# Kernel optimization log

Measured on AMD Instinct MI355X. Metric: run time of the kernel, lower is better.

Reference implementation:

```python
import jax, jax.numpy as jnp
import numpy as np

T, B, H = 2048, 64, 256   # time, batch, hidden/input/memory size
A = 256                   # attention_size
IN = H + H                # cell input size = input_size + memory_size = 512
NEG = -1e12


def setup_inputs() -> dict:
    key = jax.random.key(0)
    ks = jax.random.split(key, 12)
    s = lambda k, shape, fan: jax.random.normal(k, shape, jnp.float32) / np.sqrt(fan)
    inp = {
        "input": jax.random.normal(ks[0], (B, H), jnp.float32),
        "memory": jax.random.normal(ks[1], (T, B, H), jnp.float32),
        "memory_mask": jax.random.bernoulli(ks[2], 0.9, (T, B)),
        "state": jax.random.normal(ks[3], (B, H), jnp.float32),
        # attention MLP: Linear(input+state+memory -> A, no bias), Tanh, Linear(A -> 1, no bias)
        "W_a1": s(ks[4], (H + H + H, A), H * 3),
        "w_a2": s(ks[5], (A,), A),
        # gate: Linear(IN -> IN, no bias) + sigmoid
        "W_gate": s(ks[6], (IN, IN), IN),
        # GRUCell params (torch layout: [3H, in], gates order r,z,n)
        "W_ih": s(ks[7], (3 * H, IN), IN),
        "W_hh": s(ks[8], (3 * H, H), H),
        "b_ih": jnp.zeros((3 * H,), jnp.float32),
        "b_hh": jnp.zeros((3 * H,), jnp.float32),
    }
    return inp


def reference(input, memory, memory_mask, state, W_a1, w_a2, W_gate, W_ih, W_hh, b_ih, b_hh):
    # --- additive attention: tanh(W1 @ [input, state, memory]) @ w2 ---
    # split W_a1 by the concat layout [input | state | memory]
    qs = jnp.concatenate([input, state], axis=-1) @ W_a1[: 2 * H]      # [B, A]
    mp = jnp.einsum("tbh,ha->tba", memory, W_a1[2 * H :])               # [T, B, A]
    logits = jnp.tanh(qs[None] + mp) @ w_a2                              # [T, B]
    logits = jnp.where(memory_mask, logits, NEG)
    scores = jax.nn.softmax(logits, axis=0)                              # [T, B]
    attn_vec = jnp.einsum("tb,tbh->bh", scores, memory)                  # [B, H]

    # --- gate ---
    new_input = jnp.concatenate([input, attn_vec], axis=-1)              # [B, 2H]
    gated = new_input * jax.nn.sigmoid(new_input @ W_gate)

    # --- GRU cell (torch semantics, gates r, z, n) ---
    gi = gated @ W_ih.T + b_ih                                           # [B, 3H]
    gh = state @ W_hh.T + b_hh                                           # [B, 3H]
    i_r, i_z, i_n = jnp.split(gi, 3, axis=-1)
    h_r, h_z, h_n = jnp.split(gh, 3, axis=-1)
    r = jax.nn.sigmoid(i_r + h_r)
    z = jax.nn.sigmoid(i_z + h_z)
    n = jnp.tanh(i_n + r * h_n)
    return (1.0 - z) * n + z * state                                     # [B, H]
```

## Files before the change

kernel.cpp:

```cpp
#include <hip/hip_runtime.h>
#include <hip/hip_bf16.h>

#define B_DIM 64
#define H_DIM 256
#define NG 256
#define SUBS 8
#define RCH 64
#define NEG_INF -1e12f

typedef __attribute__((ext_vector_type(8))) short short8;
typedef __attribute__((ext_vector_type(4))) float f32x4;

__device__ __forceinline__ unsigned short bfbits(float f) {
    __hip_bfloat16 h = __float2bfloat16(f);
    unsigned short u;
    __builtin_memcpy(&u, &h, 2);
    return u;
}
__device__ __forceinline__ float fast_tanh(float x) {
    float e = __expf(2.0f * x);
    return 1.0f - 2.0f / (e + 1.0f);
}
__device__ __forceinline__ float fast_sigmoid(float x) {
    return 1.0f / (1.0f + __expf(-x));
}

__global__ void prep_qs_kernel(const float* __restrict__ W_a1,
                               const float* __restrict__ input,
                               const float* __restrict__ state,
                               unsigned short* __restrict__ WmT,
                               float* __restrict__ qs) {
    __shared__ float cat[512];
    int bid = blockIdx.x, tid = threadIdx.x;
    if (bid < 256) {
        WmT[tid * 256 + bid] = bfbits(W_a1[(512 + bid) * 256 + tid]);
    } else {
        int b = bid - 256;
        cat[tid] = input[b * 256 + tid];
        cat[256 + tid] = state[b * 256 + tid];
        __syncthreads();
        int a = tid;
        float s0 = 0.f, s1 = 0.f, s2 = 0.f, s3 = 0.f;
        #pragma unroll 4
        for (int k = 0; k < 512; k += 4) {
            s0 += cat[k]     * W_a1[(k)     * 256 + a];
            s1 += cat[k + 1] * W_a1[(k + 1) * 256 + a];
            s2 += cat[k + 2] * W_a1[(k + 2) * 256 + a];
            s3 += cat[k + 3] * W_a1[(k + 3) * 256 + a];
        }
        qs[b * 256 + a] = (s0 + s1) + (s2 + s3);
    }
}

__global__ __launch_bounds__(512, 2) void attn_kernel(
    const float* __restrict__ memory, const int* __restrict__ mask,
    const unsigned short* __restrict__ WmT,
    const float* __restrict__ qs, const float* __restrict__ w_a2,
    float* __restrict__ part_l, float* __restrict__ part_acc)
{
    extern __shared__ char smem[];
    unsigned short* slab0 = (unsigned short*)smem;
    unsigned short* slab1 = (unsigned short*)(smem + 32768);
    float* qsT   = (float*)(smem + 65536);
    float* lpart = (float*)(smem + 65536 + 66560);
    int*   maskL = (int*)(smem + 65536 + 66560 + 2048);

    int g = blockIdx.x;
    int tid = threadIdx.x;
    int lane = tid & 63, w = tid >> 6;
    int lr = lane & 15, lh = lane >> 4;
    const float* mbase = memory + (size_t)g * (512 * H_DIM);

    #pragma unroll
    for (int i = 0; i < 32; ++i) {
        int idx = i * 512 + tid;
        qsT[(idx & 255) * 65 + (idx >> 8)] = qs[idx];
    }
    maskL[tid] = mask[g * 512 + tid];

    int wa0 = w * 32;
    short8 areg[8][2];
    #pragma unroll
    for (int kk = 0; kk < 8; ++kk)
        #pragma unroll
        for (int mf = 0; mf < 2; ++mf)
            areg[kk][mf] = *(const short8*)(WmT + (wa0 + mf * 16 + lr) * 256 + kk * 32 + lh * 8);

    float wv[2][4];
    #pragma unroll
    for (int mf = 0; mf < 2; ++mf)
        #pragma unroll
        for (int r = 0; r < 4; ++r)
            wv[mf][r] = w_a2[wa0 + mf * 16 + lh * 4 + r];

    float4 ld[8];
    #pragma unroll
    for (int i = 0; i < 8; ++i)
        ld[i] = *((const float4*)(mbase + (size_t)(i * 8 + w) * H_DIM) + lane);
    int wby = (lane * 8) ^ (w << 4);
    #pragma unroll
    for (int i = 0; i < 8; ++i) {
        ushort4 o;
        o.x = bfbits(ld[i].x); o.y = bfbits(ld[i].y);
        o.z = bfbits(ld[i].z); o.w = bfbits(ld[i].w);
        *(ushort4*)((char*)slab0 + (i * 8 + w) * 512 + wby) = o;
    }
    __syncthreads();

    float a32[32];
    #pragma unroll
    for (int j = 0; j < 32; ++j) a32[j] = 0.f;
    float l_acc = 0.f;

    for (int s = 0; s < SUBS; ++s) {
        const char* cur = (const char*)((s & 1) ? slab1 : slab0);
        char* nxt = (char*)((s & 1) ? slab0 : slab1);

        if (s < SUBS - 1) {
            #pragma unroll
            for (int i = 0; i < 8; ++i)
                ld[i] = *((const float4*)(mbase + (size_t)((s + 1) * RCH + i * 8 + w) * H_DIM) + lane);
        }

        f32x4 acc[2][4];
        #pragma unroll
        for (int mf = 0; mf < 2; ++mf)
            #pragma unroll
            for (int nf = 0; nf < 4; ++nf)
                acc[mf][nf] = (f32x4){0.f, 0.f, 0.f, 0.f};
        #pragma unroll
        for (int kk = 0; kk < 8; ++kk) {
            int kbyte = kk * 64 + lh * 16;
            #pragma unroll
            for (int nf = 0; nf < 4; ++nf) {
                int t = nf * 16 + lr;
                int sw = kbyte ^ ((t & 7) << 4);
                short8 bfr = *(const short8*)(cur + t * 512 + sw);
                acc[0][nf] = __builtin_amdgcn_mfma_f32_16x16x32_bf16(areg[kk][0], bfr, acc[0][nf], 0, 0, 0);
                acc[1][nf] = __builtin_amdgcn_mfma_f32_16x16x32_bf16(areg[kk][1], bfr, acc[1][nf], 0, 0, 0);
            }
        }

        if (s < SUBS - 1) {
            #pragma unroll
            for (int i = 0; i < 8; ++i) {
                ushort4 o;
                o.x = bfbits(ld[i].x); o.y = bfbits(ld[i].y);
                o.z = bfbits(ld[i].z); o.w = bfbits(ld[i].w);
                *(ushort4*)(nxt + (i * 8 + w) * 512 + wby) = o;
            }
        }

        #pragma unroll
        for (int nf = 0; nf < 4; ++nf) {
            int brow = nf * 16 + lr;
            float sv = 0.f;
            #pragma unroll
            for (int mf = 0; mf < 2; ++mf)
                #pragma unroll
                for (int r = 0; r < 4; ++r) {
                    int a = wa0 + mf * 16 + lh * 4 + r;
                    sv += wv[mf][r] * fast_tanh(qsT[a * 65 + brow] + acc[mf][nf][r]);
                }
            sv += __shfl_xor(sv, 16);
            sv += __shfl_xor(sv, 32);
            if (lh == 0) lpart[w * 64 + brow] = sv;
        }
        __syncthreads();

        float lg = 0.f;
        #pragma unroll
        for (int ww = 0; ww < 8; ++ww) lg += lpart[ww * 64 + lane];
        float p = maskL[s * 64 + lane] ? __expf(lg) : 0.f;
        if (w == 0) l_acc += p;

        #pragma unroll
        for (int j = 0; j < 4; ++j) {
            int swb = (w * 64 + j * 16) ^ ((lane & 7) << 4);
            uint4 u = *(const uint4*)(cur + lane * 512 + swb);
            a32[j * 8 + 0] += p * __uint_as_float(u.x << 16);
            a32[j * 8 + 1] += p * __uint_as_float(u.x & 0xFFFF0000u);
            a32[j * 8 + 2] += p * __uint_as_float(u.y << 16);
            a32[j * 8 + 3] += p * __uint_as_float(u.y & 0xFFFF0000u);
            a32[j * 8 + 4] += p * __uint_as_float(u.z << 16);
            a32[j * 8 + 5] += p * __uint_as_float(u.z & 0xFFFF0000u);
            a32[j * 8 + 6] += p * __uint_as_float(u.w << 16);
            a32[j * 8 + 7] += p * __uint_as_float(u.w & 0xFFFF0000u);
        }
        __syncthreads();
    }

    float* acc2 = qsT;
    #pragma unroll
    for (int j4 = 0; j4 < 8; ++j4)
        *(float4*)(&acc2[lane * 257 + w * 32 + j4 * 4]) =
            (float4){a32[j4 * 4 + 0], a32[j4 * 4 + 1], a32[j4 * 4 + 2], a32[j4 * 4 + 3]};
    __syncthreads();
    int hh = tid & 255, bq = tid >> 8;
    for (int bb = bq; bb < 64; bb += 2)
        part_acc[((size_t)bb * NG + g) * 256 + hh] = acc2[bb * 257 + hh];
    if (w == 0) part_l[lane * NG + g] = l_acc;
}

__global__ void mergegate_kernel(const float* __restrict__ part_l,
                                 const float* __restrict__ part_acc,
                                 const float* __restrict__ input,
                                 const float* __restrict__ W_gate,
                                 float* __restrict__ gated) {
    __shared__ float ni[512];
    __shared__ float lbuf[256];
    int b = blockIdx.x, tid = threadIdx.x;
    if (tid < 256) lbuf[tid] = part_l[b * NG + tid];
    __syncthreads();
    for (int off = 128; off > 0; off >>= 1) {
        if (tid < off) lbuf[tid] += lbuf[tid + off];
        __syncthreads();
    }
    float L = lbuf[0];
    if (tid < 256) {
        ni[tid] = input[b * 256 + tid];
    } else {
        int h = tid - 256;
        const float* pa = part_acc + (size_t)b * NG * 256 + h;
        float s = 0.f;
        #pragma unroll 8
        for (int g2 = 0; g2 < NG; ++g2) s += pa[(size_t)g2 * 256];
        ni[256 + h] = s / L;
    }
    __syncthreads();
    int j = tid;
    float s0 = 0.f, s1 = 0.f, s2 = 0.f, s3 = 0.f;
    #pragma unroll 4
    for (int k = 0; k < 512; k += 4) {
        s0 += ni[k]     * W_gate[(k)     * 512 + j];
        s1 += ni[k + 1] * W_gate[(k + 1) * 512 + j];
        s2 += ni[k + 2] * W_gate[(k + 2) * 512 + j];
        s3 += ni[k + 3] * W_gate[(k + 3) * 512 + j];
    }
    float s = (s0 + s1) + (s2 + s3);
    gated[b * 512 + j] = ni[j] * fast_sigmoid(s);
}

__global__ __launch_bounds__(768) void gru_kernel(
    const float* __restrict__ gated, const float* __restrict__ state,
    const float* __restrict__ W_ih, const float* __restrict__ W_hh,
    const float* __restrict__ b_ih, const float* __restrict__ b_hh,
    float* __restrict__ out) {
    __shared__ float ld_g[4][512];
    __shared__ float ld_s[4][256];
    __shared__ float xi[3][16][4];
    __shared__ float xh[3][16][4];
    int ht = blockIdx.x & 15, bt = blockIdx.x >> 4;
    int tid = threadIdx.x;
    #pragma unroll
    for (int i = 0; i < 3; ++i) {
        int idx = i * 768 + tid;
        if (idx < 2048) ld_g[idx >> 9][idx & 511] = gated[(bt * 4 + (idx >> 9)) * 512 + (idx & 511)];
    }
    #pragma unroll
    for (int i = 0; i < 2; ++i) {
        int idx = i * 768 + tid;
        if (idx < 1024) ld_s[idx >> 8][idx & 255] = state[(bt * 4 + (idx >> 8)) * 256 + (idx & 255)];
    }

    int gid = tid >> 4, lk = tid & 15;
    int gate = gid >> 4, hl = gid & 15;
    int j = gate * 256 + ht * 16 + hl;

    float4 wi[8], wh[4];
    #pragma unroll
    for (int it = 0; it < 8; ++it)
        wi[it] = *(const float4*)(W_ih + (size_t)j * 512 + it * 64 + lk * 4);
    #pragma unroll
    for (int it = 0; it < 4; ++it)
        wh[it] = *(const float4*)(W_hh + (size_t)j * 256 + it * 64 + lk * 4);
    float bi = b_ih[j], bh = b_hh[j];
    __syncthreads();

    #pragma unroll
    for (int bb = 0; bb < 4; ++bb) {
        float g0 = 0.f, g1 = 0.f;
        #pragma unroll
        for (int it = 0; it < 8; ++it) {
            float4 gv = *(const float4*)(&ld_g[bb][it * 64 + lk * 4]);
            g0 += wi[it].x * gv.x + wi[it].z * gv.z;
            g1 += wi[it].y * gv.y + wi[it].w * gv.w;
        }
        float h0 = 0.f, h1 = 0.f;
        #pragma unroll
        for (int it = 0; it < 4; ++it) {
            float4 sv = *(const float4*)(&ld_s[bb][it * 64 + lk * 4]);
            h0 += wh[it].x * sv.x + wh[it].z * sv.z;
            h1 += wh[it].y * sv.y + wh[it].w * sv.w;
        }
        float gi_ = g0 + g1, gh_ = h0 + h1;
        #pragma unroll
        for (int m = 1; m < 16; m <<= 1) {
            gi_ += __shfl_xor(gi_, m);
            gh_ += __shfl_xor(gh_, m);
        }
        if (lk == 0) { xi[gate][hl][bb] = gi_ + bi; xh[gate][hl][bb] = gh_ + bh; }
    }
    __syncthreads();
    if (tid < 64) {
        int bb = tid >> 4, hl2 = tid & 15;
        float ir = xi[0][hl2][bb], hr = xh[0][hl2][bb];
        float iz = xi[1][hl2][bb], hz = xh[1][hl2][bb];
        float in_ = xi[2][hl2][bb], hn = xh[2][hl2][bb];
        float r = fast_sigmoid(ir + hr);
        float z = fast_sigmoid(iz + hz);
        float n = fast_tanh(in_ + r * hn);
        out[(bt * 4 + bb) * 256 + ht * 16 + hl2] =
            (1.f - z) * n + z * ld_s[bb][ht * 16 + hl2];
    }
}

extern "C" void kernel_launch(void* const* d_in, const int* in_sizes, int n_in,
                              void* d_out, int out_size, void* d_ws, size_t ws_size,
                              hipStream_t stream) {
    const float* input  = (const float*)d_in[0];
    const float* memory = (const float*)d_in[1];
    const int*   mask   = (const int*)d_in[2];
    const float* state  = (const float*)d_in[3];
    const float* W_a1   = (const float*)d_in[4];
    const float* w_a2   = (const float*)d_in[5];
    const float* W_gate = (const float*)d_in[6];
    const float* W_ih   = (const float*)d_in[7];
    const float* W_hh   = (const float*)d_in[8];
    const float* b_ih   = (const float*)d_in[9];
    const float* b_hh   = (const float*)d_in[10];
    float* out = (float*)d_out;

    char* ws = (char*)d_ws;
    unsigned short* WmT = (unsigned short*)(ws + 0);
    float* qs       = (float*)(ws + 131072);
    float* gated    = (float*)(ws + 196608);
    float* part_l   = (float*)(ws + 327680);
    float* part_acc = (float*)(ws + 393216);

    prep_qs_kernel<<<320, 256, 0, stream>>>(W_a1, input, state, WmT, qs);

    (void)hipFuncSetAttribute((const void*)attn_kernel,
                              hipFuncAttributeMaxDynamicSharedMemorySize, 136192);
    attn_kernel<<<NG, 512, 136192, stream>>>(
        memory, mask, WmT, qs, w_a2, part_l, part_acc);

    mergegate_kernel<<<64, 512, 0, stream>>>(part_l, part_acc, input, W_gate, gated);
    gru_kernel<<<256, 768, 0, stream>>>(gated, state, W_ih, W_hh, b_ih, b_hh, out);
}
```

Measured before the change: 97.93 us.

## Stream fp32 memory tiles directly to LDS via global_load_lds, repartition MFMA warps

```diff
diff --git a/kernel.cpp b/kernel.cpp
--- a/kernel.cpp
+++ b/kernel.cpp
@@ -6,10 +6,12 @@
 #define NG 256
 #define SUBS 8
 #define RCH 64
-#define NEG_INF -1e12f
 
 typedef __attribute__((ext_vector_type(8))) short short8;
 typedef __attribute__((ext_vector_type(4))) float f32x4;
+
+typedef const __attribute__((address_space(1))) void gas_void;
+typedef __attribute__((address_space(3))) void las_void;
 
 __device__ __forceinline__ unsigned short bfbits(float f) {
     __hip_bfloat16 h = __float2bfloat16(f);
@@ -52,59 +54,58 @@
     }
 }
 
-__global__ __launch_bounds__(512, 2) void attn_kernel(
+__global__ __launch_bounds__(512, 1) void attn_kernel(
     const float* __restrict__ memory, const int* __restrict__ mask,
     const unsigned short* __restrict__ WmT,
     const float* __restrict__ qs, const float* __restrict__ w_a2,
     float* __restrict__ part_l, float* __restrict__ part_acc)
 {
     extern __shared__ char smem[];
-    unsigned short* slab0 = (unsigned short*)smem;
-    unsigned short* slab1 = (unsigned short*)(smem + 32768);
-    float* qsT   = (float*)(smem + 65536);
-    float* lpart = (float*)(smem + 65536 + 66560);
-    int*   maskL = (int*)(smem + 65536 + 66560 + 2048);
+    float* lpart = (float*)(smem + 131072);
+    int*   maskL = (int*)(smem + 131072 + 1024);
 
     int g = blockIdx.x;
     int tid = threadIdx.x;
     int lane = tid & 63, w = tid >> 6;
+    int aw = w & 3, rw = w >> 2;
     int lr = lane & 15, lh = lane >> 4;
-    const float* mbase = memory + (size_t)g * (512 * H_DIM);
-
-    #pragma unroll
-    for (int i = 0; i < 32; ++i) {
-        int idx = i * 512 + tid;
-        qsT[(idx & 255) * 65 + (idx >> 8)] = qs[idx];
-    }
+    const char* mbase = (const char*)(memory) + (size_t)g * (512 * 1024);
+
     maskL[tid] = mask[g * 512 + tid];
 
-    int wa0 = w * 32;
-    short8 areg[8][2];
+    int wa0 = aw * 64;
+    short8 areg[8][4];
     #pragma unroll
     for (int kk = 0; kk < 8; ++kk)
         #pragma unroll
-        for (int mf = 0; mf < 2; ++mf)
+        for (int mf = 0; mf < 4; ++mf)
             areg[kk][mf] = *(const short8*)(WmT + (wa0 + mf * 16 + lr) * 256 + kk * 32 + lh * 8);
 
-    float wv[2][4];
-    #pragma unroll
-    for (int mf = 0; mf < 2; ++mf)
-        #pragma unroll
-        for (int r = 0; r < 4; ++r)
-            wv[mf][r] = w_a2[wa0 + mf * 16 + lh * 4 + r];
-
-    float4 ld[8];
-    #pragma unroll
-    for (int i = 0; i < 8; ++i)
-        ld[i] = *((const float4*)(mbase + (size_t)(i * 8 + w) * H_DIM) + lane);
-    int wby = (lane * 8) ^ (w << 4);
-    #pragma unroll
-    for (int i = 0; i < 8; ++i) {
-        ushort4 o;
-        o.x = bfbits(ld[i].x); o.y = bfbits(ld[i].y);
-        o.z = bfbits(ld[i].z); o.w = bfbits(ld[i].w);
-        *(ushort4*)((char*)slab0 + (i * 8 + w) * 512 + wby) = o;
-    }
+    float qv[2][4][4], wv[4][4];
+    #pragma unroll
+    for (int mf = 0; mf < 4; ++mf)
+        #pragma unroll
+        for (int r = 0; r < 4; ++r) {
+            int a = wa0 + mf * 16 + lh * 4 + r;
+            wv[mf][r] = w_a2[a];
+            #pragma unroll
+            for (int nf = 0; nf < 2; ++nf)
+                qv[nf][mf][r] = qs[(rw * 32 + nf * 16 + lr) * 256 + a];
+        }
+
+    auto stage = [&](int s) {
+        char* dst = smem + ((s & 1) << 16);
+        #pragma unroll
+        for (int i = 0; i < 8; ++i) {
+            int row = w * 8 + i;
+            const char* gp = mbase + (size_t)(s * RCH + row) * 1024
+                           + ((lane * 16) ^ (i << 4));
+            __builtin_amdgcn_global_load_lds((gas_void*)gp,
+                                             (las_void*)(dst + row * 1024), 16, 0, 0);
+        }
+    };
+
+    stage(0);
     __syncthreads();
 
     float a32[32];
@@ -113,93 +114,82 @@
     float l_acc = 0.f;
 
     for (int s = 0; s < SUBS; ++s) {
-        const char* cur = (const char*)((s & 1) ? slab1 : slab0);
-        char* nxt = (char*)((s & 1) ? slab0 : slab1);
-
-        if (s < SUBS - 1) {
+        const char* cur = smem + ((s & 1) << 16);
+        if (s < SUBS - 1) stage(s + 1);
+
+        f32x4 acc[4][2];
+        #pragma unroll
+        for (int mf = 0; mf < 4; ++mf)
             #pragma unroll
-            for (int i = 0; i < 8; ++i)
-                ld[i] = *((const float4*)(mbase + (size_t)((s + 1) * RCH + i * 8 + w) * H_DIM) + lane);
-        }
-
-        f32x4 acc[2][4];
-        #pragma unroll
-        for (int mf = 0; mf < 2; ++mf)
+            for (int nf = 0; nf < 2; ++nf)
+                acc[mf][nf] = (f32x4){0.f, 0.f, 0.f, 0.f};
+
+        #pragma unroll
+        for (int kk = 0; kk < 8; ++kk) {
             #pragma unroll
-            for (int nf = 0; nf < 4; ++nf)
-                acc[mf][nf] = (f32x4){0.f, 0.f, 0.f, 0.f};
-        #pragma unroll
-        for (int kk = 0; kk < 8; ++kk) {
-            int kbyte = kk * 64 + lh * 16;
-            #pragma unroll
-            for (int nf = 0; nf < 4; ++nf) {
-                int t = nf * 16 + lr;
-                int sw = kbyte ^ ((t & 7) << 4);
-                short8 bfr = *(const short8*)(cur + t * 512 + sw);
-                acc[0][nf] = __builtin_amdgcn_mfma_f32_16x16x32_bf16(areg[kk][0], bfr, acc[0][nf], 0, 0, 0);
-                acc[1][nf] = __builtin_amdgcn_mfma_f32_16x16x32_bf16(areg[kk][1], bfr, acc[1][nf], 0, 0, 0);
+            for (int nf = 0; nf < 2; ++nf) {
+                int row = rw * 32 + nf * 16 + lr;
+                int sw = (row & 7) << 4;
+                int base = kk * 128 + lh * 32;
+                uint4 u0 = *(const uint4*)(cur + row * 1024 + (base ^ sw));
+                uint4 u1 = *(const uint4*)(cur + row * 1024 + ((base + 16) ^ sw));
+                union { short8 s8; unsigned int u[4]; } frag;
+                frag.u[0] = __builtin_amdgcn_perm(u0.y, u0.x, 0x07060302u);
+                frag.u[1] = __builtin_amdgcn_perm(u0.w, u0.z, 0x07060302u);
+                frag.u[2] = __builtin_amdgcn_perm(u1.y, u1.x, 0x07060302u);
+                frag.u[3] = __builtin_amdgcn_perm(u1.w, u1.z, 0x07060302u);
+                #pragma unroll
+                for (int mf = 0; mf < 4; ++mf)
+                    acc[mf][nf] = __builtin_amdgcn_mfma_f32_16x16x32_bf16(
+                        areg[kk][mf], frag.s8, acc[mf][nf], 0, 0, 0);
             }
         }
 
-        if (s < SUBS - 1) {
-            #pragma unroll
-            for (int i = 0; i < 8; ++i) {
-                ushort4 o;
-                o.x = bfbits(ld[i].x); o.y = bfbits(ld[i].y);
-                o.z = bfbits(ld[i].z); o.w = bfbits(ld[i].w);
-                *(ushort4*)(nxt + (i * 8 + w) * 512 + wby) = o;
-            }
-        }
-
-        #pragma unroll
-        for (int nf = 0; nf < 4; ++nf) {
-            int brow = nf * 16 + lr;
+        #pragma unroll
+        for (int nf = 0; nf < 2; ++nf) {
             float sv = 0.f;
             #pragma unroll
-            for (int mf = 0; mf < 2; ++mf)
+            for (int mf = 0; mf < 4; ++mf)
                 #pragma unroll
-                for (int r = 0; r < 4; ++r) {
-                    int a = wa0 + mf * 16 + lh * 4 + r;
-                    sv += wv[mf][r] * fast_tanh(qsT[a * 65 + brow] + acc[mf][nf][r]);
-                }
+                for (int r = 0; r < 4; ++r)
+                    sv += wv[mf][r] * fast_tanh(qv[nf][mf][r] + acc[mf][nf][r]);
             sv += __shfl_xor(sv, 16);
             sv += __shfl_xor(sv, 32);
-            if (lh == 0) lpart[w * 64 + brow] = sv;
+            if (lh == 0) lpart[w * 32 + nf * 16 + lr] = sv;
         }
         __syncthreads();
 
         float lg = 0.f;
         #pragma unroll
-        for (int ww = 0; ww < 8; ++ww) lg += lpart[ww * 64 + lane];
+        for (int aq = 0; aq < 4; ++aq)
+            lg += lpart[((lane >> 5) * 4 + aq) * 32 + (lane & 31)];
         float p = maskL[s * 64 + lane] ? __expf(lg) : 0.f;
-        if (w == 0) l_acc += p;
-
-        #pragma unroll
-        for (int j = 0; j < 4; ++j) {
-            int swb = (w * 64 + j * 16) ^ ((lane & 7) << 4);
-            uint4 u = *(const uint4*)(cur + lane * 512 + swb);
-            a32[j * 8 + 0] += p * __uint_as_float(u.x << 16);
-            a32[j * 8 + 1] += p * __uint_as_float(u.x & 0xFFFF0000u);
-            a32[j * 8 + 2] += p * __uint_as_float(u.y << 16);
-            a32[j * 8 + 3] += p * __uint_as_float(u.y & 0xFFFF0000u);
-            a32[j * 8 + 4] += p * __uint_as_float(u.z << 16);
-            a32[j * 8 + 5] += p * __uint_as_float(u.z & 0xFFFF0000u);
-            a32[j * 8 + 6] += p * __uint_as_float(u.w << 16);
-            a32[j * 8 + 7] += p * __uint_as_float(u.w & 0xFFFF0000u);
+        l_acc += p;
+
+        #pragma unroll
+        for (int j = 0; j < 8; ++j) {
+            int off = (w * 128 + j * 16) ^ ((lane & 7) << 4);
+            float4 u = *(const float4*)(cur + lane * 1024 + off);
+            a32[j * 4 + 0] += p * u.x;
+            a32[j * 4 + 1] += p * u.y;
+            a32[j * 4 + 2] += p * u.z;
+            a32[j * 4 + 3] += p * u.w;
         }
         __syncthreads();
     }
 
-    float* acc2 = qsT;
-    #pragma unroll
-    for (int j4 = 0; j4 < 8; ++j4)
-        *(float4*)(&acc2[lane * 257 + w * 32 + j4 * 4]) =
+    float* acc2 = (float*)smem;
+    #pragma unroll
+    for (int j4 = 0; j4 < 8; ++j4) {
+        int off = ((j4 * 16) ^ ((lane & 7) << 4)) >> 2;
+        *(float4*)(&acc2[lane * 260 + w * 32 + off]) =
             (float4){a32[j4 * 4 + 0], a32[j4 * 4 + 1], a32[j4 * 4 + 2], a32[j4 * 4 + 3]};
+    }
     __syncthreads();
     int hh = tid & 255, bq = tid >> 8;
     for (int bb = bq; bb < 64; bb += 2)
-        part_acc[((size_t)bb * NG + g) * 256 + hh] = acc2[bb * 257 + hh];
-    if (w == 0) part_l[lane * NG + g] = l_acc;
+        part_acc[((size_t)g * 64 + bb) * 256 + hh] = acc2[bb * 260 + hh];
+    if (w == 0) part_l[g * 64 + lane] = l_acc;
 }
 
 __global__ void mergegate_kernel(const float* __restrict__ part_l,
@@ -210,7 +200,7 @@
     __shared__ float ni[512];
     __shared__ float lbuf[256];
     int b = blockIdx.x, tid = threadIdx.x;
-    if (tid < 256) lbuf[tid] = part_l[b * NG + tid];
+    if (tid < 256) lbuf[tid] = part_l[tid * 64 + b];
     __syncthreads();
     for (int off = 128; off > 0; off >>= 1) {
         if (tid < off) lbuf[tid] += lbuf[tid + off];
@@ -221,10 +211,10 @@
         ni[tid] = input[b * 256 + tid];
     } else {
         int h = tid - 256;
-        const float* pa = part_acc + (size_t)b * NG * 256 + h;
+        const float* pa = part_acc + (size_t)b * 256 + h;
         float s = 0.f;
         #pragma unroll 8
-        for (int g2 = 0; g2 < NG; ++g2) s += pa[(size_t)g2 * 256];
+        for (int g2 = 0; g2 < NG; ++g2) s += pa[(size_t)g2 * 64 * 256];
         ni[256 + h] = s / L;
     }
     __syncthreads();
@@ -341,8 +331,8 @@
     prep_qs_kernel<<<320, 256, 0, stream>>>(W_a1, input, state, WmT, qs);
 
     (void)hipFuncSetAttribute((const void*)attn_kernel,
-                              hipFuncAttributeMaxDynamicSharedMemorySize, 136192);
-    attn_kernel<<<NG, 512, 136192, stream>>>(
+                              hipFuncAttributeMaxDynamicSharedMemorySize, 134144);
+    attn_kernel<<<NG, 512, 134144, stream>>>(
         memory, mask, WmT, qs, w_a2, part_l, part_acc);
 
     mergegate_kernel<<<64, 512, 0, stream>>>(part_l, part_acc, input, W_gate, gated);
```

After: 159.6 us. 1.63x slower.
